# Performance work log

Hardware: AMD Instinct MI355X
Metric: run time of the kernel (lower is better)

## Reference

```python
import jax, jax.numpy as jnp
import numpy as np

N, E = 50000, 800000
IN, H1, H2, HEADS, EMB = 128, 32, 32, 4, 128
NEG_SLOPE = 0.2  # DGL GATConv default leaky_relu slope


def setup_inputs() -> dict:
    key = jax.random.key(0)
    ks = jax.random.split(key, 14)
    s = 0.05
    return {
        "x": jax.random.normal(ks[0], (N, IN), jnp.float32),
        "src": jax.random.randint(ks[1], (E,), 0, N, jnp.int32),
        "dst": jax.random.randint(ks[2], (E,), 0, N, jnp.int32),
        "W1": jax.random.normal(ks[3], (IN, HEADS * H1), jnp.float32) * s,
        "al1": jax.random.normal(ks[4], (HEADS, H1), jnp.float32) * s,
        "ar1": jax.random.normal(ks[5], (HEADS, H1), jnp.float32) * s,
        "b1": jnp.zeros((HEADS * H1,), jnp.float32),
        "W2": jax.random.normal(ks[6], (HEADS * H1, HEADS * H2), jnp.float32) * s,
        "al2": jax.random.normal(ks[7], (HEADS, H2), jnp.float32) * s,
        "ar2": jax.random.normal(ks[8], (HEADS, H2), jnp.float32) * s,
        "b2": jnp.zeros((HEADS * H2,), jnp.float32),
        "Wp": jax.random.normal(ks[9], (HEADS * H2, EMB), jnp.float32) * s,
        "bp": jnp.zeros((EMB,), jnp.float32),
    }


def gat_layer(x, W, al, ar, b, src, dst, heads, d_out):
    n = x.shape[0]
    feat = (x @ W).reshape(n, heads, d_out)            # [N,H,D]
    el = (feat * al).sum(-1)                           # [N,H]
    er = (feat * ar).sum(-1)                           # [N,H]
    e = jax.nn.leaky_relu(el[src] + er[dst], NEG_SLOPE)  # [E,H]
    # edge softmax over destination segments
    m = jax.ops.segment_max(e, dst, num_segments=n)    # [N,H] (-inf for empty)
    ex = jnp.exp(e - m[dst])                           # [E,H]
    z = jax.ops.segment_sum(ex, dst, num_segments=n)   # [N,H]
    alpha = ex / z[dst]                                # [E,H]
    msg = alpha[:, :, None] * feat[src]                # [E,H,D]
    out = jax.ops.segment_sum(msg, dst, num_segments=n)  # [N,H,D]
    return out + b.reshape(1, heads, d_out)


def reference(x, src, dst, W1, al1, ar1, b1, W2, al2, ar2, b2, Wp, bp):
    h = gat_layer(x, W1, al1, ar1, b1, src, dst, HEADS, H1).reshape(N, -1)
    h = gat_layer(h, W2, al2, ar2, b2, src, dst, HEADS, H2).reshape(N, -1)
    out = h @ Wp + bp
    return (h, out)
```

## Files before the change

kernel.cpp:

```cpp
#include <hip/hip_runtime.h>
#include <hip/hip_bf16.h>

#define N_NODES 50000
#define HEADS 4
#define DHEAD 32
#define F 128
#define NEG_SLOPE 0.2f
#define MAXD 64
#define SCH 2048
#define NCHUNK 64
#define RSZ_MAX 6256

typedef unsigned int uint;
typedef unsigned short ushort;
typedef __attribute__((ext_vector_type(8))) short bf16x8;
typedef __attribute__((ext_vector_type(4))) float f32x4;

__device__ __forceinline__ float bf2f(ushort u) {
    union { uint i; float f; } c; c.i = ((uint)u) << 16; return c.f;
}
__device__ __forceinline__ ushort f2bf(float f) {
    union { float f; uint i; } c; c.f = f;
    uint u = c.i + 0x7FFF + ((c.i >> 16) & 1);
    return (ushort)(u >> 16);
}
__device__ __forceinline__ float sel4(int h, float a, float b, float c, float d) {
    return (h & 2) ? ((h & 1) ? d : c) : ((h & 1) ? b : a);
}

__global__ __launch_bounds__(256) void hist_lds_wtrans_kernel(
    const int* __restrict__ dst, int* __restrict__ parthist,
    int* __restrict__ lrank,
    const float* __restrict__ W1, const float* __restrict__ W2,
    const float* __restrict__ Wp,
    const float* __restrict__ al1, const float* __restrict__ ar1,
    const float* __restrict__ al2, const float* __restrict__ ar2,
    ushort* __restrict__ WT, int E, int N, int CH, int RSZ) {
    __shared__ int lhist[RSZ_MAX];
    if (blockIdx.x < (uint)(8 * NCHUNK)) {
        int r = blockIdx.x & 7;
        int c = blockIdx.x >> 3;
        int nlo = r * RSZ;
        int nhi = nlo + RSZ; if (nhi > N) nhi = N;
        for (int j = threadIdx.x; j < RSZ; j += 256) lhist[j] = 0;
        __syncthreads();
        int lo = c * CH, hi = lo + CH; if (hi > E) hi = E;
        for (int i = lo + threadIdx.x; i < hi; i += 256) {
            int d = dst[i];
            if (d >= nlo && d < nhi) lrank[i] = atomicAdd(&lhist[d - nlo], 1);
        }
        __syncthreads();
        int* ph = parthist + (size_t)(r * NCHUNK + c) * RSZ;
        for (int j = threadIdx.x; j < RSZ; j += 256) ph[j] = lhist[j];
        return;
    }
    int bid = blockIdx.x - 8 * NCHUNK;
    if (bid < 3) {
        const float* W = (bid == 0) ? W1 : (bid == 1) ? W2 : Wp;
        ushort* T = WT + (size_t)bid * 128 * 128;
        for (int i = threadIdx.x; i < 128 * 128; i += 256) {
            int r = i >> 7, c = i & 127;
            T[c * 128 + r] = f2bf(W[i]);
        }
    } else {
        const float* W   = (bid == 3) ? W1 : W2;
        const float* a_l = (bid == 3) ? al1 : al2;
        const float* a_r = (bid == 3) ? ar1 : ar2;
        ushort* T = WT + 3 * 128 * 128 + (bid - 3) * 16 * 128;
        for (int i = threadIdx.x; i < 16 * 128; i += 256) {
            int c = i >> 7, k = i & 127;
            float v = 0.f;
            if (c < 8) {
                int h = c & 3;
                const float* a  = (c < 4) ? (a_l + h * 32) : (a_r + h * 32);
                const float* wr = W + k * 128 + h * 32;
#pragma unroll
                for (int d = 0; d < 32; d++) v += wr[d] * a[d];
            }
            T[i] = f2bf(v);
        }
    }
}

__global__ __launch_bounds__(256) void scanA_kernel(int* __restrict__ parthist,
                                                    int* __restrict__ local_sc,
                                                    int* __restrict__ partials,
                                                    int N, int RSZ) {
    int i = blockIdx.x * 256 + threadIdx.x;
    int deg = 0;
    if (i < N) {
        int r = i / RSZ;
        int li = i - r * RSZ;
        size_t base = (size_t)(r * NCHUNK) * RSZ + li;
        for (int c = 0; c < NCHUNK; c++) {
            size_t idx = base + (size_t)c * RSZ;
            int t = parthist[idx];
            parthist[idx] = deg;
            deg += t;
        }
    }
    int lane = threadIdx.x & 63;
    int w = threadIdx.x >> 6;
    int x = deg;
#pragma unroll
    for (int off = 1; off < 64; off <<= 1) {
        int t = __shfl_up(x, off);
        if (lane >= off) x += t;
    }
    __shared__ int wsum[4];
    if (lane == 63) wsum[w] = x;
    __syncthreads();
    int wpre = 0;
#pragma unroll
    for (int k = 0; k < 4; k++)
        if (k < w) wpre += wsum[k];
    if (i < N) local_sc[i] = x - deg + wpre;
    if (threadIdx.x == 255) partials[blockIdx.x] = wpre + x;
}

__global__ void scanB_kernel(int* __restrict__ partials, int NP) {
    int tid = threadIdx.x;
    int v = (tid < NP) ? partials[tid] : 0;
    int lane = tid & 63;
    int w = tid >> 6;
    int x = v;
#pragma unroll
    for (int off = 1; off < 64; off <<= 1) {
        int t = __shfl_up(x, off);
        if (lane >= off) x += t;
    }
    __shared__ int wsum[4];
    if (lane == 63) wsum[w] = x;
    __syncthreads();
    int wpre = 0;
#pragma unroll
    for (int k = 0; k < 4; k++)
        if (k < w) wpre += wsum[k];
    if (tid < NP) partials[tid] = x - v + wpre;
}

__global__ __launch_bounds__(256) void scanC_kernel(int* __restrict__ offs,
                                                    const int* __restrict__ partials,
                                                    int N, int E) {
    int i = blockIdx.x * 256 + threadIdx.x;
    if (i < N) offs[i] += partials[blockIdx.x];
    if (i == 0) offs[N] = E;
}

__global__ void posfix_kernel(const int* __restrict__ dst,
                              const int* __restrict__ offs,
                              const int* __restrict__ parthist,
                              int* __restrict__ lrank, int E, int CH, int RSZ) {
    int i = blockIdx.x * 256 + threadIdx.x;
    if (i < E) {
        int d = dst[i];
        int c = i / CH;
        int r = d / RSZ;
        int li = d - r * RSZ;
        lrank[i] += offs[d] + parthist[(size_t)(r * NCHUNK + c) * RSZ + li];
    }
}

__global__ __launch_bounds__(256) void scatter_ranged_kernel(
    const int* __restrict__ src, const int* __restrict__ pos,
    int* __restrict__ csr_src, int E) {
    int range = blockIdx.x & 7;
    int chunk = blockIdx.x >> 3;
    int base = chunk * SCH + threadIdx.x;
    int lo = (int)(((long long)range * E) >> 3);
    int hi = (int)(((long long)(range + 1) * E) >> 3);
#pragma unroll
    for (int k = 0; k < SCH / 256; k++) {
        int i = base + k * 256;
        if (i < E) {
            int p = pos[i];
            if (p >= lo && p < hi) csr_src[p] = src[i];
        }
    }
}

template <bool A_FP32, bool OUT_BF16, bool BIAS, bool ELER>
__global__ __launch_bounds__(256) void mfma_gemm_kernel(
    const void* __restrict__ Av, const ushort* __restrict__ BT,
    const float* __restrict__ bias, const ushort* __restrict__ ALR,
    void* __restrict__ Cv, float* __restrict__ el, float* __restrict__ er, int M) {
    int wid = threadIdx.x >> 6;
    int lane = threadIdx.x & 63;
    int row0 = blockIdx.x * 64 + wid * 16;
    int rsub = lane & 15;
    int kg = lane >> 4;
    int row = row0 + rsub;
    int rowc = (row < M) ? row : (M - 1);

    bf16x8 af[4];
    if (A_FP32) {
        const float* A = (const float*)Av;
        const float* ap = A + (size_t)rowc * 128 + kg * 8;
#pragma unroll
        for (int ks = 0; ks < 4; ks++) {
            float4 lo = *(const float4*)(ap + ks * 32);
            float4 hi = *(const float4*)(ap + ks * 32 + 4);
            bf16x8 v;
            v[0] = (short)f2bf(lo.x); v[1] = (short)f2bf(lo.y);
            v[2] = (short)f2bf(lo.z); v[3] = (short)f2bf(lo.w);
            v[4] = (short)f2bf(hi.x); v[5] = (short)f2bf(hi.y);
            v[6] = (short)f2bf(hi.z); v[7] = (short)f2bf(hi.w);
            af[ks] = v;
        }
    } else {
        const ushort* A = (const ushort*)Av;
        const ushort* ap = A + (size_t)rowc * 128 + kg * 8;
#pragma unroll
        for (int ks = 0; ks < 4; ks++) af[ks] = *(const bf16x8*)(ap + ks * 32);
    }

    f32x4 acc[8];
#pragma unroll
    for (int ct = 0; ct < 8; ct++) acc[ct] = (f32x4){0.f, 0.f, 0.f, 0.f};

    const ushort* bp = BT + (size_t)rsub * 128 + kg * 8;
#pragma unroll
    for (int ks = 0; ks < 4; ks++) {
#pragma unroll
        for (int ct = 0; ct < 8; ct++) {
            bf16x8 bf = *(const bf16x8*)(bp + (size_t)ct * 16 * 128 + ks * 32);
            acc[ct] = __builtin_amdgcn_mfma_f32_16x16x32_bf16(af[ks], bf, acc[ct], 0, 0, 0);
        }
    }

    f32x4 acce = (f32x4){0.f, 0.f, 0.f, 0.f};
    if (ELER) {
        const ushort* ep = ALR + rsub * 128 + kg * 8;
#pragma unroll
        for (int ks = 0; ks < 4; ks++) {
            bf16x8 eb = *(const bf16x8*)(ep + ks * 32);
            acce = __builtin_amdgcn_mfma_f32_16x16x32_bf16(af[ks], eb, acce, 0, 0, 0);
        }
    }

    if (row0 >= M) return;

#pragma unroll
    for (int ct = 0; ct < 8; ct++) {
        int col = ct * 16 + rsub;
        float bv = BIAS ? bias[col] : 0.f;
#pragma unroll
        for (int r = 0; r < 4; r++) {
            int gr = row0 + kg * 4 + r;
            if (gr < M) {
                float v = acc[ct][r] + bv;
                if (OUT_BF16) ((ushort*)Cv)[(size_t)gr * 128 + col] = f2bf(v);
                else          ((float*)Cv)[(size_t)gr * 128 + col] = v;
            }
        }
    }

    if (ELER && rsub < 8) {
#pragma unroll
        for (int r = 0; r < 4; r++) {
            int gr = row0 + kg * 4 + r;
            if (gr < M) {
                if (rsub < 4) el[(size_t)gr * 4 + rsub] = acce[r];
                else          er[(size_t)gr * 4 + (rsub - 4)] = acce[r];
            }
        }
    }
}

template <bool F32OUT>
__global__ __launch_bounds__(256) void aggregate_kernel(
    const ushort* __restrict__ featb, const float* __restrict__ el,
    const float* __restrict__ er, const float* __restrict__ bias,
    const int* __restrict__ offsets, const int* __restrict__ csr_src,
    void* __restrict__ outv, int N) {
    __shared__ int   s_sv[16][MAXD + 1];
    __shared__ float s_lg[16][MAXD + 1][4];
    int tid = threadIdx.x;
    int gl = tid & 15;
    int g  = tid >> 4;
    int lane = tid & 63;
    int n = blockIdx.x * 16 + g;
    if (n >= N) return;
    int start = offsets[n], end = offsets[n + 1];
    int deg = end - start;
    bool fast = (deg <= MAXD);

    float4 erv = *(const float4*)(er + (size_t)n * 4);
    float er_h[4] = {erv.x, erv.y, erv.z, erv.w};

    float m[4], s[4];
#pragma unroll
    for (int h = 0; h < 4; h++) { m[h] = -1e30f; s[h] = 0.f; }

    for (int e = start + gl; e < end; e += 16) {
        int sv = csr_src[e];
        float4 ev = *(const float4*)(el + (size_t)sv * 4);
        float elh[4] = {ev.x, ev.y, ev.z, ev.w};
        int idx = e - start;
        if (fast) s_sv[g][idx] = sv;
#pragma unroll
        for (int h = 0; h < 4; h++) {
            float v = elh[h] + er_h[h];
            v = (v >= 0.f) ? v : NEG_SLOPE * v;
            if (fast) s_lg[g][idx][h] = v;
            float mn = fmaxf(m[h], v);
            s[h] = s[h] * __expf(m[h] - mn) + __expf(v - mn);
            m[h] = mn;
        }
    }
#pragma unroll
    for (int off = 1; off < 16; off <<= 1) {
#pragma unroll
        for (int h = 0; h < 4; h++) {
            float mo = __shfl_xor(m[h], off);
            float so = __shfl_xor(s[h], off);
            float mn = fmaxf(m[h], mo);
            s[h] = s[h] * __expf(m[h] - mn) + so * __expf(mo - mn);
            m[h] = mn;
        }
    }

    int h0 = gl >> 2;
    int c0 = gl * 8;
    float acc[8] = {};

    if (fast) {
        float rz[4];
#pragma unroll
        for (int h = 0; h < 4; h++) rz[h] = (deg > 0) ? 1.0f / s[h] : 0.f;
        for (int e = gl; e < deg; e += 16) {
#pragma unroll
            for (int h = 0; h < 4; h++)
                s_lg[g][e][h] = __expf(s_lg[g][e][h] - m[h]) * rz[h];
        }
        for (int e0 = 0; e0 < deg; e0 += 8) {
            int nb = deg - e0; if (nb > 8) nb = 8;
            float av[8]; int svv[8];
#pragma unroll
            for (int jj = 0; jj < 8; jj++) {
                int idx = (jj < nb) ? (e0 + jj) : e0;
                svv[jj] = s_sv[g][idx];
                av[jj] = (jj < nb) ? s_lg[g][idx][h0] : 0.f;
            }
#pragma unroll
            for (int jj = 0; jj < 8; jj++) {
                uint4 f0 = *(const uint4*)(featb + (size_t)svv[jj] * 128 + c0);
                acc[0] = fmaf(av[jj], bf2f(f0.x & 0xFFFF), acc[0]);
                acc[1] = fmaf(av[jj], bf2f(f0.x >> 16),    acc[1]);
                acc[2] = fmaf(av[jj], bf2f(f0.y & 0xFFFF), acc[2]);
                acc[3] = fmaf(av[jj], bf2f(f0.y >> 16),    acc[3]);
                acc[4] = fmaf(av[jj], bf2f(f0.z & 0xFFFF), acc[4]);
                acc[5] = fmaf(av[jj], bf2f(f0.z >> 16),    acc[5]);
                acc[6] = fmaf(av[jj], bf2f(f0.w & 0xFFFF), acc[6]);
                acc[7] = fmaf(av[jj], bf2f(f0.w >> 16),    acc[7]);
            }
        }
    } else {
        float mh  = sel4(h0, m[0], m[1], m[2], m[3]);
        float sh  = sel4(h0, s[0], s[1], s[2], s[3]);
        float rzh = (deg > 0) ? 1.0f / sh : 0.f;
        int j = gl & 3;
        float erh = sel4(h0, er_h[0], er_h[1], er_h[2], er_h[3]);
        int bidx = lane & 60;
        for (int e = start; e < end; e += 4) {
            int rem = end - e;
            int ej = e + ((j < rem) ? j : 0);
            int svj = csr_src[ej];
            float v = el[(size_t)svj * 4 + h0] + erh;
            v = (v >= 0.f) ? v : NEG_SLOPE * v;
            float a = __expf(v - mh) * rzh;
            if (j >= rem) a = 0.f;
#pragma unroll
            for (int jj = 0; jj < 4; jj++) {
                float ajj = __shfl(a, bidx | jj);
                int svjj  = __shfl(svj, bidx | jj);
                uint4 f0 = *(const uint4*)(featb + (size_t)svjj * 128 + c0);
                acc[0] = fmaf(ajj, bf2f(f0.x & 0xFFFF), acc[0]);
                acc[1] = fmaf(ajj, bf2f(f0.x >> 16),    acc[1]);
                acc[2] = fmaf(ajj, bf2f(f0.y & 0xFFFF), acc[2]);
                acc[3] = fmaf(ajj, bf2f(f0.y >> 16),    acc[3]);
                acc[4] = fmaf(ajj, bf2f(f0.z & 0xFFFF), acc[4]);
                acc[5] = fmaf(ajj, bf2f(f0.z >> 16),    acc[5]);
                acc[6] = fmaf(ajj, bf2f(f0.w & 0xFFFF), acc[6]);
                acc[7] = fmaf(ajj, bf2f(f0.w >> 16),    acc[7]);
            }
        }
    }

    float4 b0 = *(const float4*)(bias + c0);
    float4 b1 = *(const float4*)(bias + c0 + 4);
    float o[8];
    o[0] = acc[0] + b0.x; o[1] = acc[1] + b0.y; o[2] = acc[2] + b0.z; o[3] = acc[3] + b0.w;
    o[4] = acc[4] + b1.x; o[5] = acc[5] + b1.y; o[6] = acc[6] + b1.z; o[7] = acc[7] + b1.w;
    if (F32OUT) {
        float* outf = (float*)outv;
        float4 w0, w1;
        w0.x = o[0]; w0.y = o[1]; w0.z = o[2]; w0.w = o[3];
        w1.x = o[4]; w1.y = o[5]; w1.z = o[6]; w1.w = o[7];
        *(float4*)(outf + (size_t)n * 128 + c0) = w0;
        *(float4*)(outf + (size_t)n * 128 + c0 + 4) = w1;
    } else {
        ushort* outb = (ushort*)outv;
        uint4 p;
        p.x = (uint)f2bf(o[0]) | ((uint)f2bf(o[1]) << 16);
        p.y = (uint)f2bf(o[2]) | ((uint)f2bf(o[3]) << 16);
        p.z = (uint)f2bf(o[4]) | ((uint)f2bf(o[5]) << 16);
        p.w = (uint)f2bf(o[6]) | ((uint)f2bf(o[7]) << 16);
        *(uint4*)(outb + (size_t)n * 128 + c0) = p;
    }
}

extern "C" void kernel_launch(void* const* d_in, const int* in_sizes, int n_in,
                              void* d_out, int out_size, void* d_ws, size_t ws_size,
                              hipStream_t stream) {
    const float* x   = (const float*)d_in[0];
    const int*   src = (const int*)d_in[1];
    const int*   dst = (const int*)d_in[2];
    const float* W1  = (const float*)d_in[3];
    const float* al1 = (const float*)d_in[4];
    const float* ar1 = (const float*)d_in[5];
    const float* b1  = (const float*)d_in[6];
    const float* W2  = (const float*)d_in[7];
    const float* al2 = (const float*)d_in[8];
    const float* ar2 = (const float*)d_in[9];
    const float* b2  = (const float*)d_in[10];
    const float* Wp  = (const float*)d_in[11];
    const float* bp  = (const float*)d_in[12];

    const int N = in_sizes[0] / F;
    const int E = in_sizes[1];

    float* h_out = (float*)d_out;
    float* p_out = h_out + (size_t)N * F;

    const int NB  = (N + 255) / 256;
    const int ECS = (E + SCH - 1) / SCH;
    const int CH  = (E + NCHUNK - 1) / NCHUNK;
    const int RSZ = (N + 7) / 8;

    char* w = (char*)d_ws;
    ushort* featb   = (ushort*)w;
    ushort* h1b     = featb + (size_t)N * F;
    float* el       = (float*)(h1b + (size_t)N * F);
    float* er       = el + (size_t)N * 4;
    int*   offs     = (int*)(er + (size_t)N * 4);
    int*   lrank    = offs + (N + 1);
    int*   csrsrc   = lrank + E;
    int*   partials = csrsrc + E;
    int*   parthist = partials + 256;
    ushort* WT      = (ushort*)(parthist + (size_t)8 * NCHUNK * RSZ);

    ushort* WT1  = WT;
    ushort* WT2  = WT + 128 * 128;
    ushort* WTp  = WT + 2 * 128 * 128;
    ushort* ALR1 = WT + 3 * 128 * 128;
    ushort* ALR2 = ALR1 + 16 * 128;

    hist_lds_wtrans_kernel<<<8 * NCHUNK + 5, 256, 0, stream>>>(
        dst, parthist, lrank, W1, W2, Wp, al1, ar1, al2, ar2, WT, E, N, CH, RSZ);
    scanA_kernel<<<NB, 256, 0, stream>>>(parthist, offs, partials, N, RSZ);
    scanB_kernel<<<1, 256, 0, stream>>>(partials, NB);
    scanC_kernel<<<NB, 256, 0, stream>>>(offs, partials, N, E);
    posfix_kernel<<<(E + 255) / 256, 256, 0, stream>>>(dst, offs, parthist, lrank, E, CH, RSZ);
    scatter_ranged_kernel<<<8 * ECS, 256, 0, stream>>>(src, lrank, csrsrc, E);

    int ggrid = (N + 63) / 64;
    int agrid = (N + 15) / 16;

    mfma_gemm_kernel<true, true, false, true><<<ggrid, 256, 0, stream>>>(
        x, WT1, nullptr, ALR1, featb, el, er, N);
    aggregate_kernel<false><<<agrid, 256, 0, stream>>>(
        featb, el, er, b1, offs, csrsrc, h1b, N);

    mfma_gemm_kernel<false, true, false, true><<<ggrid, 256, 0, stream>>>(
        h1b, WT2, nullptr, ALR2, featb, el, er, N);
    aggregate_kernel<true><<<agrid, 256, 0, stream>>>(
        featb, el, er, b2, offs, csrsrc, h_out, N);

    mfma_gemm_kernel<true, false, true, false><<<ggrid, 256, 0, stream>>>(
        h_out, WTp, bp, nullptr, p_out, nullptr, nullptr, N);
}
```

Baseline: 223.4 us.

## Pack per-chunk histogram counters into 16-bit and double chunk count

Degree histogram counters are packed two per 32-bit word in LDS, with packed atomicAdd, and the partial histograms and exclusive prefixes are stored as 16-bit values in global memory. This halves LDS footprint and partial-histogram traffic, and the number of edge chunks is doubled to raise parallelism in the histogram pass. The cost is a longer serial per-node loop in scanA and a 16-bit overflow risk if any node receives more than 65535 edges within one chunk or has a cumulative degree above that. RSZ=6250 is even, so the int-typed store does not clash with the next chunk.

```diff
diff --git a/kernel.cpp b/kernel.cpp
--- a/kernel.cpp
+++ b/kernel.cpp
@@ -8,7 +8,7 @@
 #define NEG_SLOPE 0.2f
 #define MAXD 64
 #define SCH 2048
-#define NCHUNK 64
+#define NCHUNK 128
 #define RSZ_MAX 6256
 
 typedef unsigned int uint;
@@ -29,29 +29,35 @@
 }
 
 __global__ __launch_bounds__(256) void hist_lds_wtrans_kernel(
-    const int* __restrict__ dst, int* __restrict__ parthist,
+    const int* __restrict__ dst, ushort* __restrict__ parthist,
     int* __restrict__ lrank,
     const float* __restrict__ W1, const float* __restrict__ W2,
     const float* __restrict__ Wp,
     const float* __restrict__ al1, const float* __restrict__ ar1,
     const float* __restrict__ al2, const float* __restrict__ ar2,
     ushort* __restrict__ WT, int E, int N, int CH, int RSZ) {
-    __shared__ int lhist[RSZ_MAX];
+    __shared__ int lhist[RSZ_MAX / 2];
     if (blockIdx.x < (uint)(8 * NCHUNK)) {
         int r = blockIdx.x & 7;
         int c = blockIdx.x >> 3;
         int nlo = r * RSZ;
         int nhi = nlo + RSZ; if (nhi > N) nhi = N;
-        for (int j = threadIdx.x; j < RSZ; j += 256) lhist[j] = 0;
+        int nw = (RSZ + 1) >> 1;
+        for (int j = threadIdx.x; j < nw; j += 256) lhist[j] = 0;
         __syncthreads();
         int lo = c * CH, hi = lo + CH; if (hi > E) hi = E;
         for (int i = lo + threadIdx.x; i < hi; i += 256) {
             int d = dst[i];
-            if (d >= nlo && d < nhi) lrank[i] = atomicAdd(&lhist[d - nlo], 1);
+            if (d >= nlo && d < nhi) {
+                int li = d - nlo;
+                int sh = (li & 1) << 4;
+                int old = atomicAdd(&lhist[li >> 1], 1 << sh);
+                lrank[i] = (old >> sh) & 0xFFFF;
+            }
         }
         __syncthreads();
-        int* ph = parthist + (size_t)(r * NCHUNK + c) * RSZ;
-        for (int j = threadIdx.x; j < RSZ; j += 256) ph[j] = lhist[j];
+        int* ph = (int*)(parthist + (size_t)(r * NCHUNK + c) * RSZ);
+        for (int j = threadIdx.x; j < nw; j += 256) ph[j] = lhist[j];
         return;
     }
     int bid = blockIdx.x - 8 * NCHUNK;
@@ -82,7 +88,7 @@
     }
 }
 
-__global__ __launch_bounds__(256) void scanA_kernel(int* __restrict__ parthist,
+__global__ __launch_bounds__(256) void scanA_kernel(ushort* __restrict__ parthist,
                                                     int* __restrict__ local_sc,
                                                     int* __restrict__ partials,
                                                     int N, int RSZ) {
@@ -95,7 +101,7 @@
         for (int c = 0; c < NCHUNK; c++) {
             size_t idx = base + (size_t)c * RSZ;
             int t = parthist[idx];
-            parthist[idx] = deg;
+            parthist[idx] = (ushort)deg;
             deg += t;
         }
     }
@@ -149,7 +155,7 @@
 
 __global__ void posfix_kernel(const int* __restrict__ dst,
                               const int* __restrict__ offs,
-                              const int* __restrict__ parthist,
+                              const ushort* __restrict__ parthist,
                               int* __restrict__ lrank, int E, int CH, int RSZ) {
     int i = blockIdx.x * 256 + threadIdx.x;
     if (i < E) {
@@ -157,7 +163,7 @@
         int c = i / CH;
         int r = d / RSZ;
         int li = d - r * RSZ;
-        lrank[i] += offs[d] + parthist[(size_t)(r * NCHUNK + c) * RSZ + li];
+        lrank[i] += offs[d] + (int)parthist[(size_t)(r * NCHUNK + c) * RSZ + li];
     }
 }
 
@@ -447,8 +453,8 @@
     int*   lrank    = offs + (N + 1);
     int*   csrsrc   = lrank + E;
     int*   partials = csrsrc + E;
-    int*   parthist = partials + 256;
-    ushort* WT      = (ushort*)(parthist + (size_t)8 * NCHUNK * RSZ);
+    ushort* parthist = (ushort*)(partials + 256);
+    ushort* WT      = parthist + (size_t)8 * NCHUNK * RSZ;
 
     ushort* WT1  = WT;
     ushort* WT2  = WT + 128 * 128;
```

Result: no change. 227.3 us (+1.8%).
